# Performance work log

Hardware: AMD Instinct MI355X
Metric: run time of the kernel (lower is better)

The kernel has to match this reference:

```python
import jax, jax.numpy as jnp
import numpy as np

DIM = 192
HEADS = 8
TIME = 256
HID = int(DIM * 2.66)  # 510
B, H, W = 4, 128, 128


def conv1x1(x, w, b):
    # w: [O, C], pointwise conv as einsum
    return jnp.einsum('bchw,oc->bohw', x, w) + b[None, :, None, None]


def dwconv3(x, w, b):
    # depthwise 3x3, w: [C, 1, 3, 3]
    y = jax.lax.conv_general_dilated(
        x, w, window_strides=(1, 1), padding='SAME',
        feature_group_count=x.shape[1],
        dimension_numbers=('NCHW', 'OIHW', 'NCHW'))
    return y + b[None, :, None, None]


def layernorm(x, w, b, eps=1e-6):
    # channel-wise LN; torch .std() is unbiased (ddof=1)
    C = x.shape[1]
    mean = x.mean(axis=1, keepdims=True)
    var = ((x - mean) ** 2).sum(axis=1, keepdims=True) / (C - 1)
    std = jnp.sqrt(var)
    return w * (x - mean) / (std + eps) + b


def modulate(x, t_emb, tw, tb):
    # time_mlp = Linear(SiLU(t_emb)); scale/shift conditioning
    t = jax.nn.silu(t_emb) @ tw.T + tb  # [B, 2C]
    scale, shift = jnp.split(t, 2, axis=-1)
    return x * (1.0 + scale[:, :, None, None]) + shift[:, :, None, None]


def l2norm(x, eps=1e-12):
    n = jnp.sqrt((x * x).sum(axis=-1, keepdims=True))
    return x / jnp.maximum(n, eps)


def mdta(x, t_emb, temp, qkv_w, qkv_b, dw_w, dw_b, proj_w, proj_b, tw, tb):
    Bn, C, Hh, Ww = x.shape
    x = modulate(x, t_emb, tw, tb)
    qkv = dwconv3(conv1x1(x, qkv_w, qkv_b), dw_w, dw_b)
    q, k, v = jnp.split(qkv, 3, axis=1)
    rs = lambda a: a.reshape(Bn, HEADS, C // HEADS, Hh * Ww)
    q, k, v = l2norm(rs(q)), l2norm(rs(k)), rs(v)
    attn = jnp.einsum('bhcl,bhdl->bhcd', q, k) * temp[None]  # [B,h,c,c]
    attn = jax.nn.softmax(attn, axis=-1)
    out = jnp.einsum('bhcd,bhdl->bhcl', attn, v).reshape(Bn, C, Hh, Ww)
    return conv1x1(out, proj_w, proj_b)


def gdfn(x, t_emb, c1_w, c1_b, dw_w, dw_b, c2_w, c2_b, tw, tb):
    x = modulate(x, t_emb, tw, tb)
    x = dwconv3(conv1x1(x, c1_w, c1_b), dw_w, dw_b)
    x1, x2 = jnp.split(x, 2, axis=1)
    return conv1x1(x1 * x2, c2_w, c2_b)


def setup_inputs() -> dict:
    key = jax.random.key(0)
    ks = jax.random.split(key, 16)
    s = 0.02
    d = {
        'x': jax.random.normal(ks[0], (B, DIM, H, W), jnp.float32),
        't_emb': jax.random.normal(ks[1], (B, TIME), jnp.float32),
        'n1_w': jnp.ones((1, DIM, 1, 1), jnp.float32),
        'n1_b': jnp.zeros((1, DIM, 1, 1), jnp.float32),
        'temp': jnp.ones((HEADS, 1, 1), jnp.float32),
        'a_qkv_w': jax.random.normal(ks[2], (3 * DIM, DIM), jnp.float32) * s,
        'a_qkv_b': jnp.zeros((3 * DIM,), jnp.float32),
        'a_dw_w': jax.random.normal(ks[3], (3 * DIM, 1, 3, 3), jnp.float32) * s,
        'a_dw_b': jnp.zeros((3 * DIM,), jnp.float32),
        'a_proj_w': jax.random.normal(ks[4], (DIM, DIM), jnp.float32) * s,
        'a_proj_b': jnp.zeros((DIM,), jnp.float32),
        'a_t_w': jax.random.normal(ks[5], (2 * DIM, TIME), jnp.float32) * s,
        'a_t_b': jnp.zeros((2 * DIM,), jnp.float32),
        'n2_w': jnp.ones((1, DIM, 1, 1), jnp.float32),
        'n2_b': jnp.zeros((1, DIM, 1, 1), jnp.float32),
        'f_c1_w': jax.random.normal(ks[6], (2 * HID, DIM), jnp.float32) * s,
        'f_c1_b': jnp.zeros((2 * HID,), jnp.float32),
        'f_dw_w': jax.random.normal(ks[7], (2 * HID, 1, 3, 3), jnp.float32) * s,
        'f_dw_b': jnp.zeros((2 * HID,), jnp.float32),
        'f_c2_w': jax.random.normal(ks[8], (DIM, HID), jnp.float32) * s,
        'f_c2_b': jnp.zeros((DIM,), jnp.float32),
        'f_t_w': jax.random.normal(ks[9], (2 * DIM, TIME), jnp.float32) * s,
        'f_t_b': jnp.zeros((2 * DIM,), jnp.float32),
    }
    return d


def reference(x, t_emb, n1_w, n1_b, temp, a_qkv_w, a_qkv_b, a_dw_w, a_dw_b,
              a_proj_w, a_proj_b, a_t_w, a_t_b, n2_w, n2_b,
              f_c1_w, f_c1_b, f_dw_w, f_dw_b, f_c2_w, f_c2_b, f_t_w, f_t_b):
    x = x + mdta(layernorm(x, n1_w, n1_b), t_emb, temp,
                 a_qkv_w, a_qkv_b, a_dw_w, a_dw_b, a_proj_w, a_proj_b, a_t_w, a_t_b)
    x = x + gdfn(layernorm(x, n2_w, n2_b), t_emb,
                 f_c1_w, f_c1_b, f_dw_w, f_dw_b, f_c2_w, f_c2_b, f_t_w, f_t_b)
    return x
```

## Files before the change

kernel.cpp:

```cpp
#include <hip/hip_runtime.h>
#include <math.h>

#define HW 16384

using short8 = __attribute__((ext_vector_type(8))) short;
using f32x4  = __attribute__((ext_vector_type(4))) float;

__device__ __forceinline__ float bf2f(unsigned short u){
  union { unsigned int i; float f; } x; x.i = ((unsigned int)u) << 16; return x.f;
}
__device__ __forceinline__ unsigned short f2bf(float f){
  union { float f; unsigned int i; } x; x.f = f;
  return (unsigned short)((x.i + 0x7FFFu + ((x.i >> 16) & 1u)) >> 16);
}

__global__ void castw_k(const float* __restrict__ in, unsigned short* __restrict__ out, int n){
  int i = blockIdx.x * 256 + threadIdx.x;
  if (i < n) out[i] = f2bf(in[i]);
}
__global__ void castw_pad_k(const float* __restrict__ in, unsigned short* __restrict__ out,
                            int M, int Kin, int Kout){
  int i = blockIdx.x * 256 + threadIdx.x;
  if (i < M * Kout){
    int m = i / Kout, k = i - m * Kout;
    out[i] = (k < Kin) ? f2bf(in[m * Kin + k]) : (unsigned short)0;
  }
}

__global__ void modk(const float* __restrict__ t_emb,
                     const float* __restrict__ aw, const float* __restrict__ ab,
                     const float* __restrict__ fw, const float* __restrict__ fb,
                     float* __restrict__ mod_a, float* __restrict__ mod_f){
  int o = blockIdx.x * 128 + threadIdx.x;
  int b = blockIdx.y;
  const float* w  = blockIdx.z ? fw : aw;
  const float* bi = blockIdx.z ? fb : ab;
  float* outp     = blockIdx.z ? mod_f : mod_a;
  const float* te = t_emb + b * 256;
  float acc = bi[o];
  for (int k = 0; k < 256; ++k){
    float u = te[k];
    float s = u / (1.f + expf(-u));
    acc += s * w[o * 256 + k];
  }
  outp[b * 384 + o] = acc;
}

__global__ __launch_bounds__(256) void lnmod_k(const float* __restrict__ x,
                                               const float* __restrict__ nw, const float* __restrict__ nb,
                                               const float* __restrict__ mod, unsigned short* __restrict__ y){
  int b = blockIdx.y;
  int t = threadIdx.x;
  int pl = t & 63, cg = t >> 6;
  int p = blockIdx.x * 64 + pl;
  const float* xb = x + (size_t)b * 192 * HW + p;
  float s = 0.f, s2 = 0.f;
  #pragma unroll 8
  for (int c = cg * 48; c < cg * 48 + 48; ++c){
    float v = xb[(size_t)c * HW]; s += v; s2 += v * v;
  }
  __shared__ float rs[4][64], rq[4][64];
  rs[cg][pl] = s; rq[cg][pl] = s2;
  __syncthreads();
  float S  = rs[0][pl] + rs[1][pl] + rs[2][pl] + rs[3][pl];
  float S2 = rq[0][pl] + rq[1][pl] + rq[2][pl] + rq[3][pl];
  float mean = S * (1.f / 192.f);
  float var  = (S2 - S * mean) * (1.f / 191.f);
  float rinv = 1.f / (sqrtf(fmaxf(var, 0.f)) + 1e-6f);
  const float* mo = mod + b * 384;
  unsigned short buf[48];
  #pragma unroll 8
  for (int i = 0; i < 48; ++i){
    int c = cg * 48 + i;
    float v = xb[(size_t)c * HW];
    float ln = nw[c] * ((v - mean) * rinv) + nb[c];
    buf[i] = f2bf(ln * (1.f + mo[c]) + mo[192 + c]);
  }
  unsigned short* yb = y + ((size_t)b * HW + p) * 192 + cg * 48;
  #pragma unroll
  for (int i = 0; i < 6; ++i) *(uint4*)(yb + i * 8) = *(const uint4*)(buf + i * 8);
}

__global__ __launch_bounds__(256) void gemm_tn(const unsigned short* __restrict__ A,
                                               const unsigned short* __restrict__ Bact,
                                               const float* __restrict__ bias,
                                               const float* resid, void* outp,
                                               int M, int K, int ofp32){
  const int N = HW;
  const unsigned short* Bp = Bact + (size_t)blockIdx.z * N * K;
  int m0 = blockIdx.x * 64, n0 = blockIdx.y * 256;
  __shared__ unsigned short As[64 * 32];
  __shared__ unsigned short Bs[256 * 32];
  int t = threadIdx.x;
  int w = t >> 6, lane = t & 63;
  int l16 = lane & 15, quad = lane >> 4;
  f32x4 z = {0.f, 0.f, 0.f, 0.f};
  f32x4 acc[4][4];
  #pragma unroll
  for (int i = 0; i < 4; ++i)
    #pragma unroll
    for (int j = 0; j < 4; ++j) acc[i][j] = z;

  int kTiles = K >> 5;
  for (int kt = 0; kt < kTiles; ++kt){
    int k0 = kt * 32;
    {
      int row = t >> 2, kc = t & 3;
      int gm = m0 + row; if (gm > M - 1) gm = M - 1;
      *(uint4*)&As[row * 32 + kc * 8] = *(const uint4*)(A + (size_t)gm * K + k0 + kc * 8);
    }
    #pragma unroll
    for (int i = 0; i < 4; ++i){
      int id = t + 256 * i;
      int row = id >> 2, kc = id & 3;
      *(uint4*)&Bs[row * 32 + kc * 8] = *(const uint4*)(Bp + (size_t)(n0 + row) * K + k0 + kc * 8);
    }
    __syncthreads();
    short8 af[4], bfr[4];
    #pragma unroll
    for (int mt = 0; mt < 4; ++mt)
      af[mt] = *(const short8*)&As[(mt * 16 + l16) * 32 + quad * 8];
    #pragma unroll
    for (int nt = 0; nt < 4; ++nt)
      bfr[nt] = *(const short8*)&Bs[(w * 64 + nt * 16 + l16) * 32 + quad * 8];
    #pragma unroll
    for (int nt = 0; nt < 4; ++nt)
      #pragma unroll
      for (int mt = 0; mt < 4; ++mt)
        acc[mt][nt] = __builtin_amdgcn_mfma_f32_16x16x32_bf16(af[mt], bfr[nt], acc[mt][nt], 0, 0, 0);
    __syncthreads();
  }
  #pragma unroll
  for (int mt = 0; mt < 4; ++mt)
    #pragma unroll
    for (int nt = 0; nt < 4; ++nt){
      int n = n0 + w * 64 + nt * 16 + l16;
      #pragma unroll
      for (int r = 0; r < 4; ++r){
        int m = m0 + mt * 16 + quad * 4 + r;
        if (m < M){
          float v = acc[mt][nt][r] + bias[m];
          size_t idx = (size_t)blockIdx.z * M * N + (size_t)m * N + n;
          if (resid) v += resid[idx];
          if (ofp32) ((float*)outp)[idx] = v;
          else       ((unsigned short*)outp)[idx] = f2bf(v);
        }
      }
    }
}

__global__ __launch_bounds__(256) void dw3_k(const unsigned short* __restrict__ in,
                                             const float* __restrict__ w, const float* __restrict__ bias,
                                             unsigned short* __restrict__ out, int C,
                                             float* __restrict__ qn, float* __restrict__ kn){
  __shared__ unsigned short tile[66 * 128];
  __shared__ float red[4];
  int zc = blockIdx.y;
  int b = zc / C, c = zc - b * C;
  int r0 = blockIdx.x * 64;
  const unsigned short* im = in + ((size_t)(b * C + c)) * HW;
  unsigned short* om = out + ((size_t)(b * C + c)) * HW;
  int t = threadIdx.x;
  #pragma unroll
  for (int i = 0; i < 5; ++i){
    int idx = t + 256 * i;
    if (idx < 1056){
      int lr = idx >> 4, lc = (idx & 15) * 8;
      int gr = r0 - 1 + lr;
      uint4 v = {0u, 0u, 0u, 0u};
      if ((unsigned)gr < 128u) v = *(const uint4*)(im + gr * 128 + lc);
      *(uint4*)&tile[lr * 128 + lc] = v;
    }
  }
  __syncthreads();
  const float* wc = w + c * 9;
  float W[9];
  #pragma unroll
  for (int i = 0; i < 9; ++i) W[i] = wc[i];
  float bs = bias[c];
  float ssq = 0.f;
  #pragma unroll
  for (int i = 0; i < 4; ++i){
    int seg = t + 256 * i;
    int orow = seg >> 4, sc = (seg & 15) * 8;
    float acc[8];
    #pragma unroll
    for (int j = 0; j < 8; ++j) acc[j] = bs;
    #pragma unroll
    for (int rr = 0; rr < 3; ++rr){
      const unsigned short* rp = &tile[(orow + rr) * 128 + sc];
      float v[10];
      v[0] = (sc > 0) ? bf2f(rp[-1]) : 0.f;
      uint4 m = *(const uint4*)rp;
      const unsigned short* mu = (const unsigned short*)&m;
      #pragma unroll
      for (int j = 0; j < 8; ++j) v[j + 1] = bf2f(mu[j]);
      v[9] = (sc < 120) ? bf2f(rp[8]) : 0.f;
      float wa = W[rr * 3], wb = W[rr * 3 + 1], wd = W[rr * 3 + 2];
      #pragma unroll
      for (int j = 0; j < 8; ++j) acc[j] += wa * v[j] + wb * v[j + 1] + wd * v[j + 2];
    }
    unsigned short ob[8];
    #pragma unroll
    for (int j = 0; j < 8; ++j){
      ob[j] = f2bf(acc[j]);
      float q = bf2f(ob[j]);
      ssq += q * q;
    }
    *(uint4*)(om + (r0 + orow) * 128 + sc) = *(uint4*)ob;
  }
  if (c < 384){
    #pragma unroll
    for (int off = 32; off; off >>= 1) ssq += __shfl_down(ssq, off);
    if ((t & 63) == 0) red[t >> 6] = ssq;
    __syncthreads();
    if (t == 0){
      float s = red[0] + red[1] + red[2] + red[3];
      float* dst = (c < 192) ? (qn + b * 192 + c) : (kn + b * 192 + c - 192);
      atomicAdd(dst, s);
    }
  }
}

__global__ __launch_bounds__(256) void dwgate_k(const unsigned short* __restrict__ h,
                                                const float* __restrict__ w, const float* __restrict__ bias,
                                                unsigned short* __restrict__ g){
  __shared__ unsigned short tile[2 * 66 * 128];
  int zc = blockIdx.y;
  int b = zc / 510, j = zc - b * 510;
  int r0 = blockIdx.x * 64;
  const unsigned short* im1 = h + ((size_t)(b * 1020 + j)) * HW;
  const unsigned short* im2 = h + ((size_t)(b * 1020 + 510 + j)) * HW;
  int t = threadIdx.x;
  #pragma unroll
  for (int i = 0; i < 9; ++i){
    int idx = t + 256 * i;
    if (idx < 2112){
      int img = (idx >= 1056) ? 1 : 0;
      int li = idx - img * 1056;
      int lr = li >> 4, lc = (li & 15) * 8;
      int gr = r0 - 1 + lr;
      uint4 v = {0u, 0u, 0u, 0u};
      const unsigned short* im = img ? im2 : im1;
      if ((unsigned)gr < 128u) v = *(const uint4*)(im + gr * 128 + lc);
      *(uint4*)&tile[img * 8448 + lr * 128 + lc] = v;
    }
  }
  __syncthreads();
  float W1[9], W2[9];
  #pragma unroll
  for (int i = 0; i < 9; ++i){ W1[i] = w[j * 9 + i]; W2[i] = w[(510 + j) * 9 + i]; }
  float b1 = bias[j], b2 = bias[510 + j];
  unsigned short* gm = g + ((size_t)(b * 510 + j)) * HW;
  #pragma unroll
  for (int i = 0; i < 4; ++i){
    int seg = t + 256 * i;
    int orow = seg >> 4, sc = (seg & 15) * 8;
    float a1[8], a2[8];
    #pragma unroll
    for (int q = 0; q < 8; ++q){ a1[q] = b1; a2[q] = b2; }
    #pragma unroll
    for (int rr = 0; rr < 3; ++rr){
      #pragma unroll
      for (int img = 0; img < 2; ++img){
        const unsigned short* rp = &tile[img * 8448 + (orow + rr) * 128 + sc];
        float v[10];
        v[0] = (sc > 0) ? bf2f(rp[-1]) : 0.f;
        uint4 m = *(const uint4*)rp;
        const unsigned short* mu = (const unsigned short*)&m;
        #pragma unroll
        for (int q = 0; q < 8; ++q) v[q + 1] = bf2f(mu[q]);
        v[9] = (sc < 120) ? bf2f(rp[8]) : 0.f;
        const float* ww = img ? W2 : W1;
        float* aa = img ? a2 : a1;
        float wa = ww[rr * 3], wb = ww[rr * 3 + 1], wd = ww[rr * 3 + 2];
        #pragma unroll
        for (int q = 0; q < 8; ++q) aa[q] += wa * v[q] + wb * v[q + 1] + wd * v[q + 2];
      }
    }
    unsigned short ob[8];
    #pragma unroll
    for (int q = 0; q < 8; ++q) ob[q] = f2bf(a1[q] * a2[q]);
    *(uint4*)(gm + (r0 + orow) * 128 + sc) = *(uint4*)ob;
  }
}

__global__ __launch_bounds__(256) void tr_k(const unsigned short* __restrict__ in,
                                            unsigned short* __restrict__ out, int C, int Kout){
  __shared__ unsigned short tile[64 * 72];
  int b = blockIdx.z;
  int p0 = blockIdx.x * 64, c0 = blockIdx.y * 64;
  int t = threadIdx.x;
  #pragma unroll
  for (int i = 0; i < 2; ++i){
    int id = t + 256 * i;
    int ch = id >> 3, pc = (id & 7) * 8;
    uint4 v = {0u, 0u, 0u, 0u};
    if (c0 + ch < C) v = *(const uint4*)(in + ((size_t)(b * C + c0 + ch)) * HW + p0 + pc);
    const unsigned short* u = (const unsigned short*)&v;
    #pragma unroll
    for (int j = 0; j < 8; ++j) tile[(pc + j) * 72 + ch] = u[j];
  }
  __syncthreads();
  #pragma unroll
  for (int i = 0; i < 2; ++i){
    int id = t + 256 * i;
    int px = id >> 3, cc = (id & 7) * 8;
    *(uint4*)(out + ((size_t)b * HW + p0 + px) * Kout + c0 + cc) = *(const uint4*)&tile[px * 72 + cc];
  }
}

__global__ __launch_bounds__(64) void qk_k(const unsigned short* __restrict__ qkv_dw, float* __restrict__ part){
  int bh = blockIdx.y; int b = bh >> 3, h = bh & 7;
  int ks = blockIdx.x;
  int lane = threadIdx.x;
  int l16 = lane & 15, quad = lane >> 4;
  const unsigned short* qb = qkv_dw + ((size_t)b * 576 + h * 24) * HW;
  const unsigned short* kb = qkv_dw + ((size_t)b * 576 + 192 + h * 24) * HW;
  f32x4 z = {0.f, 0.f, 0.f, 0.f};
  f32x4 a00 = z, a01 = z, a10 = z, a11 = z;
  for (int st = 0; st < 16; ++st){
    int k0 = ks * 512 + st * 32 + quad * 8;
    short8 qa0 = *(const short8*)(qb + (size_t)l16 * HW + k0);
    short8 qa1 = *(const short8*)(qb + (size_t)(l16 + 16) * HW + k0);
    short8 kb0 = *(const short8*)(kb + (size_t)l16 * HW + k0);
    short8 kb1 = *(const short8*)(kb + (size_t)(l16 + 16) * HW + k0);
    a00 = __builtin_amdgcn_mfma_f32_16x16x32_bf16(qa0, kb0, a00, 0, 0, 0);
    a01 = __builtin_amdgcn_mfma_f32_16x16x32_bf16(qa0, kb1, a01, 0, 0, 0);
    a10 = __builtin_amdgcn_mfma_f32_16x16x32_bf16(qa1, kb0, a10, 0, 0, 0);
    a11 = __builtin_amdgcn_mfma_f32_16x16x32_bf16(qa1, kb1, a11, 0, 0, 0);
  }
  float* pp = part + ((size_t)bh * 32 + ks) * 576;
  #pragma unroll
  for (int r = 0; r < 4; ++r){
    int c0 = quad * 4 + r, c1 = 16 + quad * 4 + r;
    int d0 = l16, d1 = 16 + l16;
    if (c0 < 24 && d0 < 24) pp[c0 * 24 + d0] = a00[r];
    if (c0 < 24 && d1 < 24) pp[c0 * 24 + d1] = a01[r];
    if (c1 < 24 && d0 < 24) pp[c1 * 24 + d0] = a10[r];
    if (c1 < 24 && d1 < 24) pp[c1 * 24 + d1] = a11[r];
  }
}

__global__ void softmax_k(const float* __restrict__ part, const float* __restrict__ qn,
                          const float* __restrict__ kn, const float* __restrict__ temp,
                          float* __restrict__ attn){
  int bh = blockIdx.x; int b = bh >> 3, h = bh & 7;
  int c = threadIdx.x;
  if (c >= 24) return;
  float tmp = temp[h];
  float qv = fmaxf(sqrtf(qn[b * 192 + h * 24 + c]), 1e-12f);
  float row[24];
  #pragma unroll
  for (int d = 0; d < 24; ++d){
    float s = 0.f;
    for (int sp = 0; sp < 32; ++sp) s += part[((size_t)bh * 32 + sp) * 576 + c * 24 + d];
    float kv = fmaxf(sqrtf(kn[b * 192 + h * 24 + d]), 1e-12f);
    row[d] = s * tmp / (qv * kv);
  }
  float mx = row[0];
  #pragma unroll
  for (int d = 1; d < 24; ++d) mx = fmaxf(mx, row[d]);
  float sum = 0.f;
  #pragma unroll
  for (int d = 0; d < 24; ++d){ row[d] = expf(row[d] - mx); sum += row[d]; }
  float inv = 1.f / sum;
  #pragma unroll
  for (int d = 0; d < 24; ++d) attn[(size_t)bh * 576 + c * 24 + d] = row[d] * inv;
}

__global__ __launch_bounds__(256) void av_k(const float* __restrict__ attn,
                                            const unsigned short* __restrict__ qkv_dw,
                                            unsigned short* __restrict__ o){
  int bh = blockIdx.y; int b = bh >> 3, h = bh & 7;
  __shared__ float As[576];
  int t = threadIdx.x;
  for (int i = t; i < 576; i += 256) As[i] = attn[(size_t)bh * 576 + i];
  __syncthreads();
  int p = blockIdx.x * 256 + t;
  const unsigned short* vb = qkv_dw + ((size_t)b * 576 + 384 + h * 24) * HW + p;
  float acc[24];
  #pragma unroll
  for (int c = 0; c < 24; ++c) acc[c] = 0.f;
  #pragma unroll
  for (int d = 0; d < 24; ++d){
    float vv = bf2f(vb[(size_t)d * HW]);
    #pragma unroll
    for (int c = 0; c < 24; ++c) acc[c] += As[c * 24 + d] * vv;
  }
  unsigned short ob[24];
  #pragma unroll
  for (int c = 0; c < 24; ++c) ob[c] = f2bf(acc[c]);
  unsigned short* op = o + ((size_t)b * HW + p) * 192 + h * 24;
  #pragma unroll
  for (int i = 0; i < 3; ++i) *(uint4*)(op + i * 8) = *(const uint4*)(ob + i * 8);
}

extern "C" void kernel_launch(void* const* d_in, const int* in_sizes, int n_in,
                              void* d_out, int out_size, void* d_ws, size_t ws_size,
                              hipStream_t stream){
  (void)in_sizes; (void)n_in; (void)out_size; (void)ws_size;
  const float* x        = (const float*)d_in[0];
  const float* t_emb    = (const float*)d_in[1];
  const float* n1_w     = (const float*)d_in[2];
  const float* n1_b     = (const float*)d_in[3];
  const float* temp     = (const float*)d_in[4];
  const float* a_qkv_w  = (const float*)d_in[5];
  const float* a_qkv_b  = (const float*)d_in[6];
  const float* a_dw_w   = (const float*)d_in[7];
  const float* a_dw_b   = (const float*)d_in[8];
  const float* a_proj_w = (const float*)d_in[9];
  const float* a_proj_b = (const float*)d_in[10];
  const float* a_t_w    = (const float*)d_in[11];
  const float* a_t_b    = (const float*)d_in[12];
  const float* n2_w     = (const float*)d_in[13];
  const float* n2_b     = (const float*)d_in[14];
  const float* f_c1_w   = (const float*)d_in[15];
  const float* f_c1_b   = (const float*)d_in[16];
  const float* f_dw_w   = (const float*)d_in[17];
  const float* f_dw_b   = (const float*)d_in[18];
  const float* f_c2_w   = (const float*)d_in[19];
  const float* f_c2_b   = (const float*)d_in[20];
  const float* f_t_w    = (const float*)d_in[21];
  const float* f_t_b    = (const float*)d_in[22];
  float* out = (float*)d_out;
  char* ws = (char*)d_ws;

  unsigned short* y_buf = (unsigned short*)(ws + 0);
  unsigned short* qkv   = (unsigned short*)(ws + 25165824);
  unsigned short* hbuf  = (unsigned short*)(ws + 25165824);
  unsigned short* gbufT = (unsigned short*)(ws + 25165824);
  unsigned short* qkvd  = (unsigned short*)(ws + 100663296);
  unsigned short* obuf  = (unsigned short*)(ws + 176160768);
  unsigned short* gbuf  = (unsigned short*)(ws + 158859264);
  const size_t S = 225705984;
  float* mod_a = (float*)(ws + S);
  float* mod_f = (float*)(ws + S + 8192);
  float* qn    = (float*)(ws + S + 16384);
  float* kn    = (float*)(ws + S + 20480);
  float* part  = (float*)(ws + S + 24576);
  float* attn  = (float*)(ws + S + 2383872);
  unsigned short* Wq  = (unsigned short*)(ws + S + 2457600);
  unsigned short* Wp  = (unsigned short*)(ws + S + 2678784);
  unsigned short* W1  = (unsigned short*)(ws + S + 2752512);
  unsigned short* W2p = (unsigned short*)(ws + S + 3144192);

  castw_k<<<dim3((110592 + 255) / 256), 256, 0, stream>>>(a_qkv_w, Wq, 110592);
  castw_k<<<dim3((36864 + 255) / 256), 256, 0, stream>>>(a_proj_w, Wp, 36864);
  castw_k<<<dim3((195840 + 255) / 256), 256, 0, stream>>>(f_c1_w, W1, 195840);
  castw_pad_k<<<dim3((98304 + 255) / 256), 256, 0, stream>>>(f_c2_w, W2p, 192, 510, 512);
  modk<<<dim3(3, 4, 2), 128, 0, stream>>>(t_emb, a_t_w, a_t_b, f_t_w, f_t_b, mod_a, mod_f);
  hipMemsetAsync(qn, 0, 2 * 768 * sizeof(float), stream);

  lnmod_k<<<dim3(256, 4), 256, 0, stream>>>(x, n1_w, n1_b, mod_a, y_buf);
  gemm_tn<<<dim3(9, 64, 4), 256, 0, stream>>>(Wq, y_buf, a_qkv_b, nullptr, qkv, 576, 192, 0);
  dw3_k<<<dim3(2, 2304), 256, 0, stream>>>(qkv, a_dw_w, a_dw_b, qkvd, 576, qn, kn);
  qk_k<<<dim3(32, 32), 64, 0, stream>>>(qkvd, part);
  softmax_k<<<32, 64, 0, stream>>>(part, qn, kn, temp, attn);
  av_k<<<dim3(64, 32), 256, 0, stream>>>(attn, qkvd, obuf);
  gemm_tn<<<dim3(3, 64, 4), 256, 0, stream>>>(Wp, obuf, a_proj_b, x, out, 192, 192, 1);

  lnmod_k<<<dim3(256, 4), 256, 0, stream>>>(out, n2_w, n2_b, mod_f, y_buf);
  gemm_tn<<<dim3(16, 64, 4), 256, 0, stream>>>(W1, y_buf, f_c1_b, nullptr, hbuf, 1020, 192, 0);
  dwgate_k<<<dim3(2, 2040), 256, 0, stream>>>(hbuf, f_dw_w, f_dw_b, gbuf);
  tr_k<<<dim3(256, 8, 4), 256, 0, stream>>>(gbuf, gbufT, 510, 512);
  gemm_tn<<<dim3(3, 64, 4), 256, 0, stream>>>(W2p, gbufT, f_c2_b, out, out, 192, 512, 1);
}
```

Baseline: 805.3 us.

## Restructure GEMMs to load activation tile once and loop over all output rows

Replaces the M×N tiled GEMM with a kernel where each block loads a 64-pixel activation strip with full K into LDS once, XOR-swizzled to avoid bank conflicts. The four waves then iterate over output-channel strips, reading weight fragments directly from global memory (cached in L2). This removes the repeated reads of the activation matrix across M-tiles and the per-k-tile syncthreads. The trade-off is large LDS use for K=512 (64 KB), which limits occupancy, and weight loads that go to global memory instead of shared memory. Some waves also get unequal work when the strip count is not a multiple of four.

```diff
diff --git a/kernel.cpp b/kernel.cpp
--- a/kernel.cpp
+++ b/kernel.cpp
@@ -81,72 +81,93 @@
   for (int i = 0; i < 6; ++i) *(uint4*)(yb + i * 8) = *(const uint4*)(buf + i * 8);
 }
 
-__global__ __launch_bounds__(256) void gemm_tn(const unsigned short* __restrict__ A,
-                                               const unsigned short* __restrict__ Bact,
-                                               const float* __restrict__ bias,
-                                               const float* resid, void* outp,
-                                               int M, int K, int ofp32){
-  const int N = HW;
-  const unsigned short* Bp = Bact + (size_t)blockIdx.z * N * K;
-  int m0 = blockIdx.x * 64, n0 = blockIdx.y * 256;
-  __shared__ unsigned short As[64 * 32];
-  __shared__ unsigned short Bs[256 * 32];
-  int t = threadIdx.x;
-  int w = t >> 6, lane = t & 63;
-  int l16 = lane & 15, quad = lane >> 4;
-  f32x4 z = {0.f, 0.f, 0.f, 0.f};
-  f32x4 acc[4][4];
-  #pragma unroll
-  for (int i = 0; i < 4; ++i)
-    #pragma unroll
-    for (int j = 0; j < 4; ++j) acc[i][j] = z;
-
-  int kTiles = K >> 5;
-  for (int kt = 0; kt < kTiles; ++kt){
-    int k0 = kt * 32;
-    {
-      int row = t >> 2, kc = t & 3;
-      int gm = m0 + row; if (gm > M - 1) gm = M - 1;
-      *(uint4*)&As[row * 32 + kc * 8] = *(const uint4*)(A + (size_t)gm * K + k0 + kc * 8);
-    }
-    #pragma unroll
-    for (int i = 0; i < 4; ++i){
-      int id = t + 256 * i;
-      int row = id >> 2, kc = id & 3;
-      *(uint4*)&Bs[row * 32 + kc * 8] = *(const uint4*)(Bp + (size_t)(n0 + row) * K + k0 + kc * 8);
-    }
-    __syncthreads();
-    short8 af[4], bfr[4];
-    #pragma unroll
-    for (int mt = 0; mt < 4; ++mt)
-      af[mt] = *(const short8*)&As[(mt * 16 + l16) * 32 + quad * 8];
-    #pragma unroll
-    for (int nt = 0; nt < 4; ++nt)
-      bfr[nt] = *(const short8*)&Bs[(w * 64 + nt * 16 + l16) * 32 + quad * 8];
-    #pragma unroll
-    for (int nt = 0; nt < 4; ++nt)
-      #pragma unroll
-      for (int mt = 0; mt < 4; ++mt)
-        acc[mt][nt] = __builtin_amdgcn_mfma_f32_16x16x32_bf16(af[mt], bfr[nt], acc[mt][nt], 0, 0, 0);
-    __syncthreads();
-  }
-  #pragma unroll
-  for (int mt = 0; mt < 4; ++mt)
-    #pragma unroll
-    for (int nt = 0; nt < 4; ++nt){
-      int n = n0 + w * 64 + nt * 16 + l16;
-      #pragma unroll
-      for (int r = 0; r < 4; ++r){
-        int m = m0 + mt * 16 + quad * 4 + r;
-        if (m < M){
-          float v = acc[mt][nt][r] + bias[m];
-          size_t idx = (size_t)blockIdx.z * M * N + (size_t)m * N + n;
-          if (resid) v += resid[idx];
-          if (ofp32) ((float*)outp)[idx] = v;
-          else       ((unsigned short*)outp)[idx] = f2bf(v);
+template<int KT, int MT>
+__global__ __launch_bounds__(256) void gemm_nmaj(const unsigned short* __restrict__ W,
+                                                 const unsigned short* __restrict__ Act,
+                                                 const float* __restrict__ bias,
+                                                 const float* resid, void* outp,
+                                                 int M, int nStrips, int ofp32){
+  constexpr int K = KT * 32;
+  constexpr int SLOTS = KT * 4;
+  __shared__ unsigned short tile[64 * K];
+  const int t = threadIdx.x;
+  const int w = t >> 6, lane = t & 63;
+  const int l16 = lane & 15, quad = lane >> 4;
+  const int b = blockIdx.y;
+  const int n0 = blockIdx.x * 64;
+  const unsigned short* actT = Act + ((size_t)b * HW + n0) * K;
+
+  uint4 v[KT];
+  #pragma unroll
+  for (int i = 0; i < KT; ++i){
+    int L = i * 256 + t;
+    v[i] = *(const uint4*)(actT + L * 8);
+  }
+  #pragma unroll
+  for (int i = 0; i < KT; ++i){
+    int L = i * 256 + t;
+    int row = L / SLOTS, slot = L - row * SLOTS;
+    int ss = slot ^ (row & 7);
+    *(uint4*)&tile[(row * SLOTS + ss) * 8] = v[i];
+  }
+  __syncthreads();
+
+  constexpr int KTU = (KT > 8) ? 4 : KT;
+  for (int s = w; s < nStrips; s += 4){
+    const int m0 = s * (MT * 16);
+    size_t woff[MT];
+    #pragma unroll
+    for (int mt = 0; mt < MT; ++mt){
+      int gm = m0 + mt * 16 + l16;
+      if (gm > M - 1) gm = M - 1;
+      woff[mt] = (size_t)gm * K + quad * 8;
+    }
+    f32x4 acc[MT][4];
+    #pragma unroll
+    for (int mt = 0; mt < MT; ++mt)
+      #pragma unroll
+      for (int nt = 0; nt < 4; ++nt) acc[mt][nt] = (f32x4){0.f, 0.f, 0.f, 0.f};
+
+    for (int k2 = 0; k2 < KT / KTU; ++k2){
+      #pragma unroll
+      for (int ki = 0; ki < KTU; ++ki){
+        const int kt = k2 * KTU + ki;
+        short8 a[MT], bf[4];
+        #pragma unroll
+        for (int mt = 0; mt < MT; ++mt)
+          a[mt] = *(const short8*)(W + woff[mt] + kt * 32);
+        #pragma unroll
+        for (int nt = 0; nt < 4; ++nt){
+          int row = nt * 16 + l16;
+          int ss = (kt * 4 + quad) ^ (row & 7);
+          bf[nt] = *(const short8*)&tile[row * K + ss * 8];
+        }
+        #pragma unroll
+        for (int nt = 0; nt < 4; ++nt)
+          #pragma unroll
+          for (int mt = 0; mt < MT; ++mt)
+            acc[mt][nt] = __builtin_amdgcn_mfma_f32_16x16x32_bf16(a[mt], bf[nt], acc[mt][nt], 0, 0, 0);
+      }
+    }
+    #pragma unroll
+    for (int mt = 0; mt < MT; ++mt){
+      #pragma unroll
+      for (int nt = 0; nt < 4; ++nt){
+        const int n = n0 + nt * 16 + l16;
+        #pragma unroll
+        for (int r = 0; r < 4; ++r){
+          int m = m0 + mt * 16 + quad * 4 + r;
+          if (m < M){
+            float vv = acc[mt][nt][r] + bias[m];
+            size_t idx = (size_t)b * M * HW + (size_t)m * HW + n;
+            if (resid) vv += resid[idx];
+            if (ofp32) ((float*)outp)[idx] = vv;
+            else       ((unsigned short*)outp)[idx] = f2bf(vv);
+          }
         }
       }
     }
+  }
 }
 
 __global__ __launch_bounds__(256) void dw3_k(const unsigned short* __restrict__ in,
@@ -453,16 +474,16 @@
   hipMemsetAsync(qn, 0, 2 * 768 * sizeof(float), stream);
 
   lnmod_k<<<dim3(256, 4), 256, 0, stream>>>(x, n1_w, n1_b, mod_a, y_buf);
-  gemm_tn<<<dim3(9, 64, 4), 256, 0, stream>>>(Wq, y_buf, a_qkv_b, nullptr, qkv, 576, 192, 0);
+  gemm_nmaj<6, 3><<<dim3(256, 4), 256, 0, stream>>>(Wq, y_buf, a_qkv_b, nullptr, qkv, 576, 12, 0);
   dw3_k<<<dim3(2, 2304), 256, 0, stream>>>(qkv, a_dw_w, a_dw_b, qkvd, 576, qn, kn);
   qk_k<<<dim3(32, 32), 64, 0, stream>>>(qkvd, part);
   softmax_k<<<32, 64, 0, stream>>>(part, qn, kn, temp, attn);
   av_k<<<dim3(64, 32), 256, 0, stream>>>(attn, qkvd, obuf);
-  gemm_tn<<<dim3(3, 64, 4), 256, 0, stream>>>(Wp, obuf, a_proj_b, x, out, 192, 192, 1);
+  gemm_nmaj<6, 3><<<dim3(256, 4), 256, 0, stream>>>(Wp, obuf, a_proj_b, x, out, 192, 4, 1);
 
   lnmod_k<<<dim3(256, 4), 256, 0, stream>>>(out, n2_w, n2_b, mod_f, y_buf);
-  gemm_tn<<<dim3(16, 64, 4), 256, 0, stream>>>(W1, y_buf, f_c1_b, nullptr, hbuf, 1020, 192, 0);
+  gemm_nmaj<6, 4><<<dim3(256, 4), 256, 0, stream>>>(W1, y_buf, f_c1_b, nullptr, hbuf, 1020, 16, 0);
   dwgate_k<<<dim3(2, 2040), 256, 0, stream>>>(hbuf, f_dw_w, f_dw_b, gbuf);
   tr_k<<<dim3(256, 8, 4), 256, 0, stream>>>(gbuf, gbufT, 510, 512);
-  gemm_tn<<<dim3(3, 64, 4), 256, 0, stream>>>(W2p, gbufT, f_c2_b, out, out, 192, 512, 1);
-}
+  gemm_nmaj<16, 3><<<dim3(256, 4), 256, 0, stream>>>(W2p, gbufT, f_c2_b, out, out, 192, 4, 1);
+}
```

Result: slower. 943.5 us (+17.2%).

## Add persistent-activation GEMM that loops over all output channels for K=192

Applied to the files above, without the earlier changes.

Adds a gemm_pn kernel that loads a 128-pixel × 192-channel activation tile into LDS once. It then iterates over every 128-row weight block, double-buffering the weight tiles. It replaces gemm_tn for the three K=192 pointwise convs (qkv, proj, GDFN first conv), so activations are read once per block instead of once per M-tile. The trade-off is a grid of only 512 blocks with large LDS use (about 64KB), which lowers parallelism and occupancy, and the epilogue does strided scalar stores.

```diff
diff --git a/kernel.cpp b/kernel.cpp
--- a/kernel.cpp
+++ b/kernel.cpp
@@ -79,6 +79,108 @@
   unsigned short* yb = y + ((size_t)b * HW + p) * 192 + cg * 48;
   #pragma unroll
   for (int i = 0; i < 6; ++i) *(uint4*)(yb + i * 8) = *(const uint4*)(buf + i * 8);
+}
+
+__global__ __launch_bounds__(256) void gemm_pn(const unsigned short* __restrict__ W,
+                                               const unsigned short* __restrict__ Act,
+                                               const float* __restrict__ bias,
+                                               const float* resid, void* outp,
+                                               int M, int nMi, int ofp32){
+  __shared__ unsigned short Bs[128 * 192];
+  __shared__ unsigned short As[2][128 * 32];
+  const int t = threadIdx.x;
+  const int lane = t & 63, w = t >> 6;
+  const int l16 = lane & 15, quad = lane >> 4;
+  const int mh = w >> 1, nh = w & 1;
+  const int b = blockIdx.y;
+  const int p0 = blockIdx.x * 128;
+  const unsigned short* actP = Act + ((size_t)b * HW + p0) * 192;
+
+  #pragma unroll
+  for (int i = 0; i < 12; ++i){
+    int c = t + 256 * i;
+    uint4 v = *(const uint4*)(actP + c * 8);
+    int row = c / 24, slot = c - row * 24;
+    *(uint4*)&Bs[row * 192 + ((slot ^ (row & 7)) * 8)] = v;
+  }
+  #pragma unroll
+  for (int i = 0; i < 2; ++i){
+    int c = t + 256 * i;
+    int row = c >> 2, kc = c & 3;
+    int gm = row; if (gm > M - 1) gm = M - 1;
+    uint4 v = *(const uint4*)(W + (size_t)gm * 192 + kc * 8);
+    *(uint4*)&As[0][row * 32 + ((kc ^ (row & 3)) * 8)] = v;
+  }
+  __syncthreads();
+
+  const int total = nMi * 6;
+  for (int mi = 0; mi < nMi; ++mi){
+    f32x4 acc[4][4];
+    #pragma unroll
+    for (int i = 0; i < 4; ++i)
+      #pragma unroll
+      for (int j = 0; j < 4; ++j) acc[i][j] = (f32x4){0.f, 0.f, 0.f, 0.f};
+
+    #pragma unroll
+    for (int kt = 0; kt < 6; ++kt){
+      const int g = mi * 6 + kt;
+      const bool more = (g + 1 < total);
+      const int nmi = (kt == 5) ? mi + 1 : mi;
+      const int nkt = (kt == 5) ? 0 : kt + 1;
+      uint4 r0, r1;
+      if (more){
+        int c0 = t,        row0 = c0 >> 2, kc0 = c0 & 3;
+        int c1 = t + 256,  row1 = c1 >> 2, kc1 = c1 & 3;
+        int gm0 = nmi * 128 + row0; if (gm0 > M - 1) gm0 = M - 1;
+        int gm1 = nmi * 128 + row1; if (gm1 > M - 1) gm1 = M - 1;
+        r0 = *(const uint4*)(W + (size_t)gm0 * 192 + nkt * 32 + kc0 * 8);
+        r1 = *(const uint4*)(W + (size_t)gm1 * 192 + nkt * 32 + kc1 * 8);
+      }
+      const unsigned short* Ab = As[kt & 1];
+      short8 af[4], bfr[4];
+      #pragma unroll
+      for (int mt = 0; mt < 4; ++mt){
+        int row = mh * 64 + mt * 16 + l16;
+        af[mt] = *(const short8*)&Ab[row * 32 + (((quad ^ (l16 & 3))) * 8)];
+      }
+      #pragma unroll
+      for (int nt = 0; nt < 4; ++nt){
+        int row = nh * 64 + nt * 16 + l16;
+        bfr[nt] = *(const short8*)&Bs[row * 192 + (((kt * 4 + quad) ^ (l16 & 7)) * 8)];
+      }
+      #pragma unroll
+      for (int nt = 0; nt < 4; ++nt)
+        #pragma unroll
+        for (int mt = 0; mt < 4; ++mt)
+          acc[mt][nt] = __builtin_amdgcn_mfma_f32_16x16x32_bf16(af[mt], bfr[nt], acc[mt][nt], 0, 0, 0);
+      if (more){
+        unsigned short* Aw = (unsigned short*)As[(kt + 1) & 1];
+        int row0 = t >> 2, kc0 = t & 3;
+        *(uint4*)&Aw[row0 * 32 + ((kc0 ^ (row0 & 3)) * 8)] = r0;
+        int c1 = t + 256, row1 = c1 >> 2, kc1 = c1 & 3;
+        *(uint4*)&Aw[row1 * 32 + ((kc1 ^ (row1 & 3)) * 8)] = r1;
+      }
+      __syncthreads();
+    }
+    const int m0 = mi * 128 + mh * 64;
+    #pragma unroll
+    for (int mt = 0; mt < 4; ++mt)
+      #pragma unroll
+      for (int nt = 0; nt < 4; ++nt){
+        int n = p0 + nh * 64 + nt * 16 + l16;
+        #pragma unroll
+        for (int r = 0; r < 4; ++r){
+          int m = m0 + mt * 16 + quad * 4 + r;
+          if (m < M){
+            float vv = acc[mt][nt][r] + bias[m];
+            size_t idx = (size_t)b * M * HW + (size_t)m * HW + n;
+            if (resid) vv += resid[idx];
+            if (ofp32) ((float*)outp)[idx] = vv;
+            else       ((unsigned short*)outp)[idx] = f2bf(vv);
+          }
+        }
+      }
+  }
 }
 
 __global__ __launch_bounds__(256) void gemm_tn(const unsigned short* __restrict__ A,
@@ -453,15 +555,15 @@
   hipMemsetAsync(qn, 0, 2 * 768 * sizeof(float), stream);
 
   lnmod_k<<<dim3(256, 4), 256, 0, stream>>>(x, n1_w, n1_b, mod_a, y_buf);
-  gemm_tn<<<dim3(9, 64, 4), 256, 0, stream>>>(Wq, y_buf, a_qkv_b, nullptr, qkv, 576, 192, 0);
+  gemm_pn<<<dim3(128, 4), 256, 0, stream>>>(Wq, y_buf, a_qkv_b, nullptr, qkv, 576, 5, 0);
   dw3_k<<<dim3(2, 2304), 256, 0, stream>>>(qkv, a_dw_w, a_dw_b, qkvd, 576, qn, kn);
   qk_k<<<dim3(32, 32), 64, 0, stream>>>(qkvd, part);
   softmax_k<<<32, 64, 0, stream>>>(part, qn, kn, temp, attn);
   av_k<<<dim3(64, 32), 256, 0, stream>>>(attn, qkvd, obuf);
-  gemm_tn<<<dim3(3, 64, 4), 256, 0, stream>>>(Wp, obuf, a_proj_b, x, out, 192, 192, 1);
+  gemm_pn<<<dim3(128, 4), 256, 0, stream>>>(Wp, obuf, a_proj_b, x, out, 192, 2, 1);
 
   lnmod_k<<<dim3(256, 4), 256, 0, stream>>>(out, n2_w, n2_b, mod_f, y_buf);
-  gemm_tn<<<dim3(16, 64, 4), 256, 0, stream>>>(W1, y_buf, f_c1_b, nullptr, hbuf, 1020, 192, 0);
+  gemm_pn<<<dim3(128, 4), 256, 0, stream>>>(W1, y_buf, f_c1_b, nullptr, hbuf, 1020, 8, 0);
   dwgate_k<<<dim3(2, 2040), 256, 0, stream>>>(hbuf, f_dw_w, f_dw_b, gbuf);
   tr_k<<<dim3(256, 8, 4), 256, 0, stream>>>(gbuf, gbufT, 510, 512);
   gemm_tn<<<dim3(3, 64, 4), 256, 0, stream>>>(W2p, gbufT, f_c2_b, out, out, 192, 512, 1);
```

After: 827.6 us. 1.03x slower.

## Double-buffer GEMM LDS tiles, XOR-swizzle LDS, and remap blocks across XCDs

Applied to the files above, without the earlier changes.

Rewrites the bf16 MFMA GEMM to prefetch the next K tile from global memory into registers while computing the current one, using two LDS buffers so only one barrier is needed per iteration. LDS column chunks are XOR-swizzled by row to reduce bank conflicts on the short8 fragment reads. The 3D grid is flattened to 1D and block ids are permuted in groups of 8, so neighbouring tiles that share activation rows land on the same XCD's L2. The cost is twice the LDS and more live registers, which may lower occupancy.

```diff
diff --git a/kernel.cpp b/kernel.cpp
--- a/kernel.cpp
+++ b/kernel.cpp
@@ -81,55 +81,86 @@
   for (int i = 0; i < 6; ++i) *(uint4*)(yb + i * 8) = *(const uint4*)(buf + i * 8);
 }
 
-__global__ __launch_bounds__(256) void gemm_tn(const unsigned short* __restrict__ A,
-                                               const unsigned short* __restrict__ Bact,
-                                               const float* __restrict__ bias,
-                                               const float* resid, void* outp,
-                                               int M, int K, int ofp32){
+__global__ __launch_bounds__(256) void gemm_tn2(const unsigned short* __restrict__ A,
+                                                const unsigned short* __restrict__ Bact,
+                                                const float* __restrict__ bias,
+                                                const float* resid, void* outp,
+                                                int M, int K, int nMb, int ofp32){
   const int N = HW;
-  const unsigned short* Bp = Bact + (size_t)blockIdx.z * N * K;
-  int m0 = blockIdx.x * 64, n0 = blockIdx.y * 256;
-  __shared__ unsigned short As[64 * 32];
-  __shared__ unsigned short Bs[256 * 32];
-  int t = threadIdx.x;
-  int w = t >> 6, lane = t & 63;
-  int l16 = lane & 15, quad = lane >> 4;
-  f32x4 z = {0.f, 0.f, 0.f, 0.f};
+  __shared__ unsigned short As[2][64 * 32];
+  __shared__ unsigned short Bs[2][256 * 32];
+  const int G = gridDim.x;
+  const int bid = blockIdx.x;
+  const int lb = (bid & 7) * (G >> 3) + (bid >> 3);
+  const int mb = lb % nMb;
+  const int rest = lb / nMb;
+  const int n0 = (rest & 63) * 256;
+  const int bz = rest >> 6;
+  const unsigned short* Bp = Bact + (size_t)bz * N * K;
+  const int m0 = mb * 64;
+  const int t = threadIdx.x;
+  const int w = t >> 6, lane = t & 63;
+  const int l16 = lane & 15, quad = lane >> 4;
+
+  const int arow = t >> 2, akc = t & 3;
+  int gm = m0 + arow; if (gm > M - 1) gm = M - 1;
+  const unsigned short* agp = A + (size_t)gm * K + akc * 8;
+  const int aoff = arow * 32 + ((akc ^ (arow & 3)) * 8);
+  const int brow = t >> 2, bkc = t & 3;
+  const unsigned short* bgp = Bp + (size_t)(n0 + brow) * K + bkc * 8;
+  const int bslot = (bkc ^ (brow & 3)) * 8;
+
   f32x4 acc[4][4];
   #pragma unroll
   for (int i = 0; i < 4; ++i)
     #pragma unroll
-    for (int j = 0; j < 4; ++j) acc[i][j] = z;
-
-  int kTiles = K >> 5;
+    for (int j = 0; j < 4; ++j) acc[i][j] = (f32x4){0.f, 0.f, 0.f, 0.f};
+
+  const int kTiles = K >> 5;
+  {
+    uint4 va = *(const uint4*)agp;
+    *(uint4*)&As[0][aoff] = va;
+    #pragma unroll
+    for (int i = 0; i < 4; ++i){
+      uint4 vb = *(const uint4*)(bgp + (size_t)(64 * i) * K);
+      *(uint4*)&Bs[0][(brow + 64 * i) * 32 + bslot] = vb;
+    }
+  }
+  __syncthreads();
+
+  const int fs = (quad ^ (l16 & 3)) * 8;
   for (int kt = 0; kt < kTiles; ++kt){
-    int k0 = kt * 32;
-    {
-      int row = t >> 2, kc = t & 3;
-      int gm = m0 + row; if (gm > M - 1) gm = M - 1;
-      *(uint4*)&As[row * 32 + kc * 8] = *(const uint4*)(A + (size_t)gm * K + k0 + kc * 8);
-    }
-    #pragma unroll
-    for (int i = 0; i < 4; ++i){
-      int id = t + 256 * i;
-      int row = id >> 2, kc = id & 3;
-      *(uint4*)&Bs[row * 32 + kc * 8] = *(const uint4*)(Bp + (size_t)(n0 + row) * K + k0 + kc * 8);
-    }
-    __syncthreads();
+    const int cur = kt & 1;
+    const bool more = (kt + 1 < kTiles);
+    uint4 va; uint4 vb[4];
+    if (more){
+      const int k0 = (kt + 1) * 32;
+      va = *(const uint4*)(agp + k0);
+      #pragma unroll
+      for (int i = 0; i < 4; ++i)
+        vb[i] = *(const uint4*)(bgp + (size_t)(64 * i) * K + k0);
+    }
     short8 af[4], bfr[4];
     #pragma unroll
     for (int mt = 0; mt < 4; ++mt)
-      af[mt] = *(const short8*)&As[(mt * 16 + l16) * 32 + quad * 8];
+      af[mt] = *(const short8*)&As[cur][(mt * 16 + l16) * 32 + fs];
     #pragma unroll
     for (int nt = 0; nt < 4; ++nt)
-      bfr[nt] = *(const short8*)&Bs[(w * 64 + nt * 16 + l16) * 32 + quad * 8];
+      bfr[nt] = *(const short8*)&Bs[cur][(w * 64 + nt * 16 + l16) * 32 + fs];
     #pragma unroll
     for (int nt = 0; nt < 4; ++nt)
       #pragma unroll
       for (int mt = 0; mt < 4; ++mt)
         acc[mt][nt] = __builtin_amdgcn_mfma_f32_16x16x32_bf16(af[mt], bfr[nt], acc[mt][nt], 0, 0, 0);
+    if (more){
+      *(uint4*)&As[cur ^ 1][aoff] = va;
+      #pragma unroll
+      for (int i = 0; i < 4; ++i)
+        *(uint4*)&Bs[cur ^ 1][(brow + 64 * i) * 32 + bslot] = vb[i];
+    }
     __syncthreads();
   }
+
   #pragma unroll
   for (int mt = 0; mt < 4; ++mt)
     #pragma unroll
@@ -140,7 +171,7 @@
         int m = m0 + mt * 16 + quad * 4 + r;
         if (m < M){
           float v = acc[mt][nt][r] + bias[m];
-          size_t idx = (size_t)blockIdx.z * M * N + (size_t)m * N + n;
+          size_t idx = (size_t)bz * M * N + (size_t)m * N + n;
           if (resid) v += resid[idx];
           if (ofp32) ((float*)outp)[idx] = v;
           else       ((unsigned short*)outp)[idx] = f2bf(v);
@@ -453,16 +484,16 @@
   hipMemsetAsync(qn, 0, 2 * 768 * sizeof(float), stream);
 
   lnmod_k<<<dim3(256, 4), 256, 0, stream>>>(x, n1_w, n1_b, mod_a, y_buf);
-  gemm_tn<<<dim3(9, 64, 4), 256, 0, stream>>>(Wq, y_buf, a_qkv_b, nullptr, qkv, 576, 192, 0);
+  gemm_tn2<<<2304, 256, 0, stream>>>(Wq, y_buf, a_qkv_b, nullptr, qkv, 576, 192, 9, 0);
   dw3_k<<<dim3(2, 2304), 256, 0, stream>>>(qkv, a_dw_w, a_dw_b, qkvd, 576, qn, kn);
   qk_k<<<dim3(32, 32), 64, 0, stream>>>(qkvd, part);
   softmax_k<<<32, 64, 0, stream>>>(part, qn, kn, temp, attn);
   av_k<<<dim3(64, 32), 256, 0, stream>>>(attn, qkvd, obuf);
-  gemm_tn<<<dim3(3, 64, 4), 256, 0, stream>>>(Wp, obuf, a_proj_b, x, out, 192, 192, 1);
+  gemm_tn2<<<768, 256, 0, stream>>>(Wp, obuf, a_proj_b, x, out, 192, 192, 3, 1);
 
   lnmod_k<<<dim3(256, 4), 256, 0, stream>>>(out, n2_w, n2_b, mod_f, y_buf);
-  gemm_tn<<<dim3(16, 64, 4), 256, 0, stream>>>(W1, y_buf, f_c1_b, nullptr, hbuf, 1020, 192, 0);
+  gemm_tn2<<<4096, 256, 0, stream>>>(W1, y_buf, f_c1_b, nullptr, hbuf, 1020, 192, 16, 0);
   dwgate_k<<<dim3(2, 2040), 256, 0, stream>>>(hbuf, f_dw_w, f_dw_b, gbuf);
   tr_k<<<dim3(256, 8, 4), 256, 0, stream>>>(gbuf, gbufT, 510, 512);
-  gemm_tn<<<dim3(3, 64, 4), 256, 0, stream>>>(W2p, gbufT, f_c2_b, out, out, 192, 512, 1);
-}
+  gemm_tn2<<<768, 256, 0, stream>>>(W2p, gbufT, f_c2_b, out, out, 192, 512, 3, 1);
+}
```

Result: slower. 907.8 us (+12.7%).
